# Performance work log

Measured on AMD Instinct MI355X. Metric: run time of the kernel, lower is better.

The kernel has to match this reference:

```python
import jax, jax.numpy as jnp
import numpy as np

B, T, C, H = 2, 2048, 1024, 16
D = C // H

def setup_inputs() -> dict:
    key = jax.random.key(0)
    ks = jax.random.split(key, 8)
    s = 1.0 / np.sqrt(C)
    return {
        "x": jax.random.normal(ks[0], (B, T, C), dtype=jnp.float32),
        "Wk": jax.random.normal(ks[1], (C, C), dtype=jnp.float32) * s,
        "Wq": jax.random.normal(ks[2], (C, C), dtype=jnp.float32) * s,
        "bq": jax.random.normal(ks[3], (C,), dtype=jnp.float32) * 0.02,
        "Wv": jax.random.normal(ks[4], (C, C), dtype=jnp.float32) * s,
        "bv": jax.random.normal(ks[5], (C,), dtype=jnp.float32) * 0.02,
        "Wo": jax.random.normal(ks[6], (C, C), dtype=jnp.float32) * s,
        "bo": jax.random.normal(ks[7], (C,), dtype=jnp.float32) * 0.02,
    }

def reference(x, Wk, Wq, bq, Wv, bv, Wo, bo):
    b, t, c = x.shape
    # projections (key has no bias, matching nn.Linear(bias=False))
    q = (x @ Wq.T + bq).reshape(b, t, H, D).transpose(0, 2, 1, 3)  # [B,H,T,D]
    k = (x @ Wk.T).reshape(b, t, H, D).transpose(0, 2, 1, 3)
    v = (x @ Wv.T + bv).reshape(b, t, H, D).transpose(0, 2, 1, 3)
    scale = D ** -0.5
    attn = jnp.einsum('bhqd,bhkd->bhqk', q, k) * scale  # [B,H,T,T]
    causal = jnp.tril(jnp.ones((t, t), dtype=bool))
    attn = jnp.where(causal[None, None], attn, -jnp.inf)
    attn = jax.nn.softmax(attn, axis=-1)
    y = jnp.einsum('bhqk,bhkd->bhqd', attn, v)  # [B,H,T,D]
    y = y.transpose(0, 2, 1, 3).reshape(b, t, c)
    return y @ Wo.T + bo
```

## Files before the change

### kernel.cpp

```cpp
#include <hip/hip_runtime.h>
#include <hip/hip_bf16.h>
#include <stdint.h>

#define B_ 2
#define T_ 2048
#define C_ 1024
#define H_ 16
#define D_ 64
#define M_ (B_ * T_)

typedef __bf16 bf16x8 __attribute__((ext_vector_type(8)));
typedef float f32x4 __attribute__((ext_vector_type(4)));
typedef float f32x16 __attribute__((ext_vector_type(16)));

__device__ inline void gload_lds16(const void* g, void* l) {
  __builtin_amdgcn_global_load_lds(
      (const __attribute__((address_space(1))) void*)g,
      (__attribute__((address_space(3))) void*)l, 16, 0, 0);
}

__global__ __launch_bounds__(256) void cvt_all(
    const float* __restrict__ x, const float* __restrict__ Wq,
    const float* __restrict__ Wk, const float* __restrict__ Wv,
    const float* __restrict__ Wo, __hip_bfloat16* __restrict__ xb,
    __hip_bfloat16* __restrict__ wqb, __hip_bfloat16* __restrict__ wkb,
    __hip_bfloat16* __restrict__ wvb, __hip_bfloat16* __restrict__ wob) {
  size_t t = (size_t)blockIdx.x * 256 + threadIdx.x;
  size_t e = t * 4;
  const float* src;
  __hip_bfloat16* dst;
  size_t off;
  if (e < 4194304) {
    src = x; dst = xb; off = e;
  } else {
    size_t u = e - 4194304;
    int seg = (int)(u >> 20);
    off = u & 1048575;
    src = (seg == 0) ? Wq : (seg == 1) ? Wk : (seg == 2) ? Wv : Wo;
    dst = (seg == 0) ? wqb : (seg == 1) ? wkb : (seg == 2) ? wvb : wob;
  }
  float4 v = *(const float4*)(src + off);
  union { __hip_bfloat16 h[4]; ushort4 u4; } cv;
  cv.h[0] = __float2bfloat16(v.x);
  cv.h[1] = __float2bfloat16(v.y);
  cv.h[2] = __float2bfloat16(v.z);
  cv.h[3] = __float2bfloat16(v.w);
  *(ushort4*)(dst + off) = cv.u4;
}

__global__ __launch_bounds__(256) void gemm_qkv(
    const __hip_bfloat16* __restrict__ X,
    const __hip_bfloat16* __restrict__ Wq,
    const __hip_bfloat16* __restrict__ Wk,
    const __hip_bfloat16* __restrict__ Wv,
    const float* __restrict__ bq, const float* __restrict__ bv,
    __hip_bfloat16* __restrict__ Qo, __hip_bfloat16* __restrict__ Ko,
    __hip_bfloat16* __restrict__ VTo) {
  const int z = blockIdx.z;
  const int bx = ((blockIdx.x & 3) << 3) | (blockIdx.x >> 2);
  const __hip_bfloat16* Amat;
  const __hip_bfloat16* Bmat;
  int bm, bn;
  if (z == 2) {
    Amat = Wv; Bmat = X; bm = blockIdx.y; bn = bx;
  } else {
    Amat = X; Bmat = (z == 0) ? Wq : Wk; bm = bx; bn = blockIdx.y;
  }

  const int tid = threadIdx.x;
  const int w = tid >> 6, lane = tid & 63;
  const int wr = w >> 1, wc = w & 1;
  const int lrow = lane & 15, lk = (lane >> 4) * 8;

  __shared__ __hip_bfloat16 As[128 * 32];
  __shared__ __hip_bfloat16 Bs[128 * 32];

  f32x4 acc[4][4];
#pragma unroll
  for (int m = 0; m < 4; ++m)
#pragma unroll
    for (int n = 0; n < 4; ++n) acc[m][n] = (f32x4){0.f, 0.f, 0.f, 0.f};

  for (int k0 = 0; k0 < C_; k0 += 32) {
#pragma unroll
    for (int it = 0; it < 2; ++it) {
      int e = it * 2048 + w * 512 + lane * 8;
      int row = e >> 5, col = e & 31;
      gload_lds16(Amat + (size_t)(bm * 128 + row) * C_ + k0 + col, &As[e]);
      gload_lds16(Bmat + (size_t)(bn * 128 + row) * C_ + k0 + col, &Bs[e]);
    }
    asm volatile("s_waitcnt vmcnt(0)" ::: "memory");
    __syncthreads();

    bf16x8 af[4], bfr[4];
#pragma unroll
    for (int m = 0; m < 4; ++m)
      af[m] = *(const bf16x8*)&As[(wr * 64 + m * 16 + lrow) * 32 + lk];
#pragma unroll
    for (int n = 0; n < 4; ++n)
      bfr[n] = *(const bf16x8*)&Bs[(wc * 64 + n * 16 + lrow) * 32 + lk];
#pragma unroll
    for (int m = 0; m < 4; ++m)
#pragma unroll
      for (int n = 0; n < 4; ++n)
        acc[m][n] = __builtin_amdgcn_mfma_f32_16x16x32_bf16(af[m], bfr[n],
                                                            acc[m][n], 0, 0, 0);
    __syncthreads();
  }

#pragma unroll
  for (int m = 0; m < 4; ++m) {
#pragma unroll
    for (int n = 0; n < 4; ++n) {
      f32x4 v = acc[m][n];
      int rowm = bm * 128 + wr * 64 + m * 16 + (lane >> 4) * 4;
      int coln = bn * 128 + wc * 64 + n * 16 + (lane & 15);
      if (z == 2) {
        int b = coln >> 11, tl = coln & 2047;
#pragma unroll
        for (int r = 0; r < 4; ++r) {
          int rc = rowm + r;
          int h = rc >> 6, d = rc & 63;
          VTo[(((size_t)(b * H_ + h)) * D_ + d) * T_ + tl] =
              __float2bfloat16(v[r] + bv[rc]);
        }
      } else {
        float bb = (z == 0) ? bq[coln] : 0.f;
        float sc = (z == 0) ? 0.18033688011112042f : 1.0f;
        int h = coln >> 6, d = coln & 63;
        __hip_bfloat16* Out = (z == 0) ? Qo : Ko;
#pragma unroll
        for (int r = 0; r < 4; ++r) {
          int row = rowm + r;
          int b = row >> 11, t = row & 2047;
          Out[(((size_t)(b * H_ + h)) * T_ + t) * D_ + d] =
              __float2bfloat16((v[r] + bb) * sc);
        }
      }
    }
  }
}

__global__ __launch_bounds__(256) void gemm_out(
    const __hip_bfloat16* __restrict__ X,
    const __hip_bfloat16* __restrict__ W,
    const float* __restrict__ bias, float* __restrict__ Out) {
  const int bm = ((blockIdx.x & 3) << 3) | (blockIdx.x >> 2);
  const int bn = blockIdx.y;
  const int tid = threadIdx.x;
  const int w = tid >> 6, lane = tid & 63;
  const int wr = w >> 1, wc = w & 1;
  const int lrow = lane & 15, lk = (lane >> 4) * 8;

  __shared__ __hip_bfloat16 As[128 * 32];
  __shared__ __hip_bfloat16 Bs[128 * 32];

  f32x4 acc[4][4];
#pragma unroll
  for (int m = 0; m < 4; ++m)
#pragma unroll
    for (int n = 0; n < 4; ++n) acc[m][n] = (f32x4){0.f, 0.f, 0.f, 0.f};

  for (int k0 = 0; k0 < C_; k0 += 32) {
#pragma unroll
    for (int it = 0; it < 2; ++it) {
      int e = it * 2048 + w * 512 + lane * 8;
      int row = e >> 5, col = e & 31;
      gload_lds16(X + (size_t)(bm * 128 + row) * C_ + k0 + col, &As[e]);
      gload_lds16(W + (size_t)(bn * 128 + row) * C_ + k0 + col, &Bs[e]);
    }
    asm volatile("s_waitcnt vmcnt(0)" ::: "memory");
    __syncthreads();

    bf16x8 af[4], bfr[4];
#pragma unroll
    for (int m = 0; m < 4; ++m)
      af[m] = *(const bf16x8*)&As[(wr * 64 + m * 16 + lrow) * 32 + lk];
#pragma unroll
    for (int n = 0; n < 4; ++n)
      bfr[n] = *(const bf16x8*)&Bs[(wc * 64 + n * 16 + lrow) * 32 + lk];
#pragma unroll
    for (int m = 0; m < 4; ++m)
#pragma unroll
      for (int n = 0; n < 4; ++n)
        acc[m][n] = __builtin_amdgcn_mfma_f32_16x16x32_bf16(af[m], bfr[n],
                                                            acc[m][n], 0, 0, 0);
    __syncthreads();
  }

#pragma unroll
  for (int m = 0; m < 4; ++m) {
#pragma unroll
    for (int n = 0; n < 4; ++n) {
      f32x4 v = acc[m][n];
      int coln = bn * 128 + wc * 64 + n * 16 + (lane & 15);
      float bb = bias[coln];
#pragma unroll
      for (int r = 0; r < 4; ++r) {
        int row = bm * 128 + wr * 64 + m * 16 + (lane >> 4) * 4 + r;
        Out[(size_t)row * C_ + coln] = v[r] + bb;
      }
    }
  }
}

#define MASKV_ -1e30f
#define MFLOOR_ -30000.0f
#define THR2_ 11.54f

__global__ __launch_bounds__(512, 2) void attn_fwd(
    const __hip_bfloat16* __restrict__ Q, const __hip_bfloat16* __restrict__ K,
    const __hip_bfloat16* __restrict__ VT, __hip_bfloat16* __restrict__ Y) {
  const int bh = blockIdx.x;
  const int j = blockIdx.y;
  const int tid = threadIdx.x;
  const int wid = tid >> 6, lane = tid & 63;
  const int g = wid >> 2, wq = wid & 3;
  const int hi = lane >> 5, q32 = lane & 31;
  const size_t base = (size_t)bh * T_ * D_;
  const int b = bh >> 4, hh = bh & 15;

  __shared__ __hip_bfloat16 Ks[2][2][64][64];
  __shared__ __hip_bfloat16 Vts[2][2][64][64];
  __shared__ float Sml[2][4][2][32];
  __shared__ float Om[4][32][68];

  const int gt = tid & 255;
  const int srow = gt >> 3, scnk = gt & 7;
  const int swz = (scnk ^ (srow & 7)) * 8;

#define STAGE(buf, kt)                                                      \
  {                                                                         \
    _Pragma("unroll") for (int h2 = 0; h2 < 2; ++h2) {                      \
      int row = srow + 32 * h2;                                             \
      gload_lds16(K + base + (size_t)((kt)*64 + row) * D_ + swz,            \
                  &Ks[g][(buf)][row][scnk * 8]);                            \
      gload_lds16(VT + base + (size_t)row * T_ + (kt)*64 + swz,             \
                  &Vts[g][(buf)][row][scnk * 8]);                           \
    }                                                                       \
  }

  for (int ph = 0; ph < 2; ++ph) {
    const int qt = ph ? (15 - j) : j;
    const int qg = qt * 128 + wq * 32 + q32;

    bf16x8 qf[4];
#pragma unroll
    for (int dk = 0; dk < 4; ++dk)
      qf[dk] = *(const bf16x8*)&Q[base + (size_t)qg * D_ + dk * 16 + hi * 8];

    f32x16 o0 = {}, o1 = {};
    float m_run = MFLOOR_, l_run = 0.f;

    STAGE(0, g);
    asm volatile("s_waitcnt vmcnt(0)" ::: "memory");
    __syncthreads();

    int cur = 0;
    for (int s = 0; s <= qt; ++s) {
      const int kt = 2 * s + g;
      if (s < qt) STAGE(cur ^ 1, 2 * (s + 1) + g);

      f32x16 st0 = {}, st1 = {};
      __builtin_amdgcn_s_setprio(1);
#pragma unroll
      for (int dk = 0; dk < 4; ++dk) {
        int off = (dk * 16 + hi * 8) ^ ((lane & 7) << 3);
        bf16x8 a0 = *(const bf16x8*)&Ks[g][cur][q32][off];
        bf16x8 a1 = *(const bf16x8*)&Ks[g][cur][q32 + 32][off];
        st0 = __builtin_amdgcn_mfma_f32_32x32x16_bf16(a0, qf[dk], st0, 0, 0, 0);
        st1 = __builtin_amdgcn_mfma_f32_32x32x16_bf16(a1, qf[dk], st1, 0, 0, 0);
      }
      __builtin_amdgcn_s_setprio(0);

      float sc[32];
#pragma unroll
      for (int r = 0; r < 16; ++r) {
        sc[r] = st0[r];
        sc[16 + r] = st1[r];
      }
      if (s == qt) {
#pragma unroll
        for (int r = 0; r < 16; ++r) {
          int kvl = (r & 3) + 8 * (r >> 2) + 4 * hi;
          if (kt * 64 + kvl > qg) sc[r] = MASKV_;
          if (kt * 64 + 32 + kvl > qg) sc[16 + r] = MASKV_;
        }
      }
      float mt = sc[0];
#pragma unroll
      for (int r = 1; r < 32; ++r) mt = fmaxf(mt, sc[r]);
      mt = fmaxf(mt, __shfl_xor(mt, 32));
      if (__any(mt - m_run > THR2_)) {
        float m_new = fmaxf(m_run, mt);
        float alpha = __builtin_exp2f(m_run - m_new);
        m_run = m_new;
        l_run *= alpha;
#pragma unroll
        for (int r = 0; r < 16; ++r) {
          o0[r] *= alpha;
          o1[r] *= alpha;
        }
      }
      float ls = 0.f;
#pragma unroll
      for (int r = 0; r < 32; ++r) {
        float p = __builtin_exp2f(sc[r] - m_run);
        sc[r] = p;
        ls += p;
      }
      ls += __shfl_xor(ls, 32);
      l_run += ls;

      __builtin_amdgcn_s_setprio(1);
#pragma unroll
      for (int ks = 0; ks < 4; ++ks) {
        union { unsigned w[4]; bf16x8 v; } pa;
        unsigned A, Bb;
        asm("v_cvt_pk_bf16_f32 %0, %1, %2"
            : "=v"(A) : "v"(sc[ks * 8 + 0]), "v"(sc[ks * 8 + 1]));
        asm("v_cvt_pk_bf16_f32 %0, %1, %2"
            : "=v"(Bb) : "v"(sc[ks * 8 + 4]), "v"(sc[ks * 8 + 5]));
        asm volatile("v_permlane32_swap_b32 %0, %1" : "+v"(A), "+v"(Bb));
        pa.w[0] = A;
        pa.w[2] = Bb;
        asm("v_cvt_pk_bf16_f32 %0, %1, %2"
            : "=v"(A) : "v"(sc[ks * 8 + 2]), "v"(sc[ks * 8 + 3]));
        asm("v_cvt_pk_bf16_f32 %0, %1, %2"
            : "=v"(Bb) : "v"(sc[ks * 8 + 6]), "v"(sc[ks * 8 + 7]));
        asm volatile("v_permlane32_swap_b32 %0, %1" : "+v"(A), "+v"(Bb));
        pa.w[1] = A;
        pa.w[3] = Bb;

        int voff = (ks * 16 + hi * 8) ^ ((lane & 7) << 3);
        bf16x8 v0 = *(const bf16x8*)&Vts[g][cur][q32][voff];
        bf16x8 v1 = *(const bf16x8*)&Vts[g][cur][q32 + 32][voff];
        o0 = __builtin_amdgcn_mfma_f32_32x32x16_bf16(v0, pa.v, o0, 0, 0, 0);
        o1 = __builtin_amdgcn_mfma_f32_32x32x16_bf16(v1, pa.v, o1, 0, 0, 0);
      }
      __builtin_amdgcn_s_setprio(0);

      asm volatile("s_waitcnt vmcnt(0)" ::: "memory");
      __syncthreads();
      cur ^= 1;
    }

    if (lane < 32) {
      Sml[g][wq][0][lane] = m_run;
      Sml[g][wq][1][lane] = l_run;
    }
    __syncthreads();
    float mo = Sml[1 - g][wq][0][q32];
    float lo_ = Sml[1 - g][wq][1][q32];
    float mstar = fmaxf(m_run, mo);
    float f = __builtin_exp2f(m_run - mstar);
    float fo = __builtin_exp2f(mo - mstar);
    float lstar = l_run * f + lo_ * fo;

    if (g == 1) {
#pragma unroll
      for (int dt = 0; dt < 2; ++dt) {
#pragma unroll
        for (int grp = 0; grp < 4; ++grp) {
          int dbase = grp * 8 + hi * 4 + dt * 32;
          float4 t4;
          t4.x = (dt ? o1[grp * 4 + 0] : o0[grp * 4 + 0]) * f;
          t4.y = (dt ? o1[grp * 4 + 1] : o0[grp * 4 + 1]) * f;
          t4.z = (dt ? o1[grp * 4 + 2] : o0[grp * 4 + 2]) * f;
          t4.w = (dt ? o1[grp * 4 + 3] : o0[grp * 4 + 3]) * f;
          *(float4*)&Om[wq][q32][dbase] = t4;
        }
      }
    }
    __syncthreads();
    if (g == 0) {
      float inv = 1.0f / lstar;
#pragma unroll
      for (int dt = 0; dt < 2; ++dt) {
#pragma unroll
        for (int grp = 0; grp < 4; ++grp) {
          int dbase = grp * 8 + hi * 4 + dt * 32;
          float4 m4 = *(float4*)&Om[wq][q32][dbase];
          union { __hip_bfloat16 h4[4]; ushort4 u; } pk;
          float e0 = (dt ? o1[grp * 4 + 0] : o0[grp * 4 + 0]) * f + m4.x;
          float e1 = (dt ? o1[grp * 4 + 1] : o0[grp * 4 + 1]) * f + m4.y;
          float e2 = (dt ? o1[grp * 4 + 2] : o0[grp * 4 + 2]) * f + m4.z;
          float e3 = (dt ? o1[grp * 4 + 3] : o0[grp * 4 + 3]) * f + m4.w;
          pk.h4[0] = __float2bfloat16(e0 * inv);
          pk.h4[1] = __float2bfloat16(e1 * inv);
          pk.h4[2] = __float2bfloat16(e2 * inv);
          pk.h4[3] = __float2bfloat16(e3 * inv);
          *(ushort4*)&Y[((size_t)b * T_ + qg) * C_ + hh * 64 + dbase] = pk.u;
        }
      }
    }
    __syncthreads();
  }
}

extern "C" void kernel_launch(void* const* d_in, const int* in_sizes, int n_in,
                              void* d_out, int out_size, void* d_ws,
                              size_t ws_size, hipStream_t stream) {
  const float* x = (const float*)d_in[0];
  const float* Wk = (const float*)d_in[1];
  const float* Wq = (const float*)d_in[2];
  const float* bq = (const float*)d_in[3];
  const float* Wv = (const float*)d_in[4];
  const float* bv = (const float*)d_in[5];
  const float* Wo = (const float*)d_in[6];
  const float* bo = (const float*)d_in[7];
  float* out = (float*)d_out;

  char* ws = (char*)d_ws;
  __hip_bfloat16* xb = (__hip_bfloat16*)(ws);
  __hip_bfloat16* wqb = (__hip_bfloat16*)(ws + (8ull << 20));
  __hip_bfloat16* wkb = (__hip_bfloat16*)(ws + (10ull << 20));
  __hip_bfloat16* wvb = (__hip_bfloat16*)(ws + (12ull << 20));
  __hip_bfloat16* wob = (__hip_bfloat16*)(ws + (14ull << 20));
  __hip_bfloat16* Qb = (__hip_bfloat16*)(ws + (16ull << 20));
  __hip_bfloat16* Kb = (__hip_bfloat16*)(ws + (24ull << 20));
  __hip_bfloat16* VTb = (__hip_bfloat16*)(ws + (32ull << 20));
  __hip_bfloat16* Yb = (__hip_bfloat16*)(ws + (40ull << 20));

  cvt_all<<<8192, 256, 0, stream>>>(x, Wq, Wk, Wv, Wo, xb, wqb, wkb, wvb, wob);
  gemm_qkv<<<dim3(32, 8, 3), 256, 0, stream>>>(xb, wqb, wkb, wvb, bq, bv, Qb,
                                               Kb, VTb);
  attn_fwd<<<dim3(32, 8), 512, 0, stream>>>(Qb, Kb, VTb, Yb);
  gemm_out<<<dim3(32, 8), 256, 0, stream>>>(Yb, wob, bo, out);
}
```

Baseline: 111.9 us.

## Deepen GEMM K-tiles with swizzled LDS and simplify attention to one tile per block

Both GEMM kernels now stage 64-wide K slices into LDS with an XOR swizzle and run two MFMA sub-steps per barrier. This halves the number of synchronisations and global-to-LDS rounds and avoids LDS bank conflicts. The attention kernel drops the two-group split-K design with its paired query tiles and LDS merge. Instead it launches 512 blocks of 256 threads, each handling one query tile with heavy tiles scheduled first, so the cross-group merge and its barriers disappear. In exchange, load balance now depends on the scheduler taking longest-first ordering, and each block walks the full causal KV range serially.

```diff
diff --git a/kernel.cpp b/kernel.cpp
--- a/kernel.cpp
+++ b/kernel.cpp
@@ -72,8 +72,8 @@
   const int wr = w >> 1, wc = w & 1;
   const int lrow = lane & 15, lk = (lane >> 4) * 8;
 
-  __shared__ __hip_bfloat16 As[128 * 32];
-  __shared__ __hip_bfloat16 Bs[128 * 32];
+  __shared__ __hip_bfloat16 As[128 * 64];
+  __shared__ __hip_bfloat16 Bs[128 * 64];
 
   f32x4 acc[4][4];
 #pragma unroll
@@ -81,30 +81,39 @@
 #pragma unroll
     for (int n = 0; n < 4; ++n) acc[m][n] = (f32x4){0.f, 0.f, 0.f, 0.f};
 
-  for (int k0 = 0; k0 < C_; k0 += 32) {
-#pragma unroll
-    for (int it = 0; it < 2; ++it) {
-      int e = it * 2048 + w * 512 + lane * 8;
-      int row = e >> 5, col = e & 31;
-      gload_lds16(Amat + (size_t)(bm * 128 + row) * C_ + k0 + col, &As[e]);
-      gload_lds16(Bmat + (size_t)(bn * 128 + row) * C_ + k0 + col, &Bs[e]);
+  const int scnk = tid & 7;
+  for (int k0 = 0; k0 < C_; k0 += 64) {
+#pragma unroll
+    for (int it = 0; it < 4; ++it) {
+      int e = it * 2048 + tid * 8;
+      int row = e >> 6;
+      int scol = (scnk ^ (row & 7)) * 8;
+      gload_lds16(Amat + (size_t)(bm * 128 + row) * C_ + k0 + scol, &As[e]);
+      gload_lds16(Bmat + (size_t)(bn * 128 + row) * C_ + k0 + scol, &Bs[e]);
     }
     asm volatile("s_waitcnt vmcnt(0)" ::: "memory");
     __syncthreads();
 
-    bf16x8 af[4], bfr[4];
-#pragma unroll
-    for (int m = 0; m < 4; ++m)
-      af[m] = *(const bf16x8*)&As[(wr * 64 + m * 16 + lrow) * 32 + lk];
-#pragma unroll
-    for (int n = 0; n < 4; ++n)
-      bfr[n] = *(const bf16x8*)&Bs[(wc * 64 + n * 16 + lrow) * 32 + lk];
-#pragma unroll
-    for (int m = 0; m < 4; ++m)
-#pragma unroll
-      for (int n = 0; n < 4; ++n)
-        acc[m][n] = __builtin_amdgcn_mfma_f32_16x16x32_bf16(af[m], bfr[n],
-                                                            acc[m][n], 0, 0, 0);
+#pragma unroll
+    for (int ks = 0; ks < 2; ++ks) {
+      bf16x8 af[4], bfr[4];
+#pragma unroll
+      for (int m = 0; m < 4; ++m) {
+        int R = wr * 64 + m * 16 + lrow;
+        af[m] = *(const bf16x8*)&As[R * 64 + ((ks * 32 + lk) ^ ((R & 7) << 3))];
+      }
+#pragma unroll
+      for (int n = 0; n < 4; ++n) {
+        int R = wc * 64 + n * 16 + lrow;
+        bfr[n] = *(const bf16x8*)&Bs[R * 64 + ((ks * 32 + lk) ^ ((R & 7) << 3))];
+      }
+#pragma unroll
+      for (int m = 0; m < 4; ++m)
+#pragma unroll
+        for (int n = 0; n < 4; ++n)
+          acc[m][n] = __builtin_amdgcn_mfma_f32_16x16x32_bf16(
+              af[m], bfr[n], acc[m][n], 0, 0, 0);
+    }
     __syncthreads();
   }
 
@@ -152,8 +161,8 @@
   const int wr = w >> 1, wc = w & 1;
   const int lrow = lane & 15, lk = (lane >> 4) * 8;
 
-  __shared__ __hip_bfloat16 As[128 * 32];
-  __shared__ __hip_bfloat16 Bs[128 * 32];
+  __shared__ __hip_bfloat16 As[128 * 64];
+  __shared__ __hip_bfloat16 Bs[128 * 64];
 
   f32x4 acc[4][4];
 #pragma unroll
@@ -161,30 +170,39 @@
 #pragma unroll
     for (int n = 0; n < 4; ++n) acc[m][n] = (f32x4){0.f, 0.f, 0.f, 0.f};
 
-  for (int k0 = 0; k0 < C_; k0 += 32) {
-#pragma unroll
-    for (int it = 0; it < 2; ++it) {
-      int e = it * 2048 + w * 512 + lane * 8;
-      int row = e >> 5, col = e & 31;
-      gload_lds16(X + (size_t)(bm * 128 + row) * C_ + k0 + col, &As[e]);
-      gload_lds16(W + (size_t)(bn * 128 + row) * C_ + k0 + col, &Bs[e]);
+  const int scnk = tid & 7;
+  for (int k0 = 0; k0 < C_; k0 += 64) {
+#pragma unroll
+    for (int it = 0; it < 4; ++it) {
+      int e = it * 2048 + tid * 8;
+      int row = e >> 6;
+      int scol = (scnk ^ (row & 7)) * 8;
+      gload_lds16(X + (size_t)(bm * 128 + row) * C_ + k0 + scol, &As[e]);
+      gload_lds16(W + (size_t)(bn * 128 + row) * C_ + k0 + scol, &Bs[e]);
     }
     asm volatile("s_waitcnt vmcnt(0)" ::: "memory");
     __syncthreads();
 
-    bf16x8 af[4], bfr[4];
-#pragma unroll
-    for (int m = 0; m < 4; ++m)
-      af[m] = *(const bf16x8*)&As[(wr * 64 + m * 16 + lrow) * 32 + lk];
-#pragma unroll
-    for (int n = 0; n < 4; ++n)
-      bfr[n] = *(const bf16x8*)&Bs[(wc * 64 + n * 16 + lrow) * 32 + lk];
-#pragma unroll
-    for (int m = 0; m < 4; ++m)
-#pragma unroll
-      for (int n = 0; n < 4; ++n)
-        acc[m][n] = __builtin_amdgcn_mfma_f32_16x16x32_bf16(af[m], bfr[n],
-                                                            acc[m][n], 0, 0, 0);
+#pragma unroll
+    for (int ks = 0; ks < 2; ++ks) {
+      bf16x8 af[4], bfr[4];
+#pragma unroll
+      for (int m = 0; m < 4; ++m) {
+        int R = wr * 64 + m * 16 + lrow;
+        af[m] = *(const bf16x8*)&As[R * 64 + ((ks * 32 + lk) ^ ((R & 7) << 3))];
+      }
+#pragma unroll
+      for (int n = 0; n < 4; ++n) {
+        int R = wc * 64 + n * 16 + lrow;
+        bfr[n] = *(const bf16x8*)&Bs[R * 64 + ((ks * 32 + lk) ^ ((R & 7) << 3))];
+      }
+#pragma unroll
+      for (int m = 0; m < 4; ++m)
+#pragma unroll
+        for (int n = 0; n < 4; ++n)
+          acc[m][n] = __builtin_amdgcn_mfma_f32_16x16x32_bf16(
+              af[m], bfr[n], acc[m][n], 0, 0, 0);
+    }
     __syncthreads();
   }
 
@@ -208,25 +226,21 @@
 #define MFLOOR_ -30000.0f
 #define THR2_ 11.54f
 
-__global__ __launch_bounds__(512, 2) void attn_fwd(
+__global__ __launch_bounds__(256, 4) void attn_fwd(
     const __hip_bfloat16* __restrict__ Q, const __hip_bfloat16* __restrict__ K,
     const __hip_bfloat16* __restrict__ VT, __hip_bfloat16* __restrict__ Y) {
-  const int bh = blockIdx.x;
-  const int j = blockIdx.y;
+  const int bh = blockIdx.x & 31;
+  const int qt = 15 - (blockIdx.x >> 5);
   const int tid = threadIdx.x;
-  const int wid = tid >> 6, lane = tid & 63;
-  const int g = wid >> 2, wq = wid & 3;
+  const int wq = tid >> 6, lane = tid & 63;
   const int hi = lane >> 5, q32 = lane & 31;
   const size_t base = (size_t)bh * T_ * D_;
   const int b = bh >> 4, hh = bh & 15;
 
-  __shared__ __hip_bfloat16 Ks[2][2][64][64];
-  __shared__ __hip_bfloat16 Vts[2][2][64][64];
-  __shared__ float Sml[2][4][2][32];
-  __shared__ float Om[4][32][68];
-
-  const int gt = tid & 255;
-  const int srow = gt >> 3, scnk = gt & 7;
+  __shared__ __hip_bfloat16 Ks[2][64][64];
+  __shared__ __hip_bfloat16 Vts[2][64][64];
+
+  const int srow = tid >> 3, scnk = tid & 7;
   const int swz = (scnk ^ (srow & 7)) * 8;
 
 #define STAGE(buf, kt)                                                      \
@@ -234,167 +248,131 @@
     _Pragma("unroll") for (int h2 = 0; h2 < 2; ++h2) {                      \
       int row = srow + 32 * h2;                                             \
       gload_lds16(K + base + (size_t)((kt)*64 + row) * D_ + swz,            \
-                  &Ks[g][(buf)][row][scnk * 8]);                            \
+                  &Ks[(buf)][row][scnk * 8]);                               \
       gload_lds16(VT + base + (size_t)row * T_ + (kt)*64 + swz,             \
-                  &Vts[g][(buf)][row][scnk * 8]);                           \
+                  &Vts[(buf)][row][scnk * 8]);                              \
     }                                                                       \
   }
 
-  for (int ph = 0; ph < 2; ++ph) {
-    const int qt = ph ? (15 - j) : j;
-    const int qg = qt * 128 + wq * 32 + q32;
-
-    bf16x8 qf[4];
-#pragma unroll
-    for (int dk = 0; dk < 4; ++dk)
-      qf[dk] = *(const bf16x8*)&Q[base + (size_t)qg * D_ + dk * 16 + hi * 8];
-
-    f32x16 o0 = {}, o1 = {};
-    float m_run = MFLOOR_, l_run = 0.f;
-
-    STAGE(0, g);
+  const int qg = qt * 128 + wq * 32 + q32;
+
+  bf16x8 qf[4];
+#pragma unroll
+  for (int dk = 0; dk < 4; ++dk)
+    qf[dk] = *(const bf16x8*)&Q[base + (size_t)qg * D_ + dk * 16 + hi * 8];
+
+  f32x16 o0 = {}, o1 = {};
+  float m_run = MFLOOR_, l_run = 0.f;
+
+  STAGE(0, 0);
+  asm volatile("s_waitcnt vmcnt(0)" ::: "memory");
+  __syncthreads();
+
+  const int nkt = 2 * qt + 2;
+  for (int kt = 0; kt < nkt; ++kt) {
+    const int cur = kt & 1;
+    if (kt + 1 < nkt) STAGE(cur ^ 1, kt + 1);
+
+    f32x16 st0 = {}, st1 = {};
+    __builtin_amdgcn_s_setprio(1);
+#pragma unroll
+    for (int dk = 0; dk < 4; ++dk) {
+      int off = (dk * 16 + hi * 8) ^ ((lane & 7) << 3);
+      bf16x8 a0 = *(const bf16x8*)&Ks[cur][q32][off];
+      bf16x8 a1 = *(const bf16x8*)&Ks[cur][q32 + 32][off];
+      st0 = __builtin_amdgcn_mfma_f32_32x32x16_bf16(a0, qf[dk], st0, 0, 0, 0);
+      st1 = __builtin_amdgcn_mfma_f32_32x32x16_bf16(a1, qf[dk], st1, 0, 0, 0);
+    }
+    __builtin_amdgcn_s_setprio(0);
+
+    float sc[32];
+#pragma unroll
+    for (int r = 0; r < 16; ++r) {
+      sc[r] = st0[r];
+      sc[16 + r] = st1[r];
+    }
+    if (kt >= 2 * qt) {
+#pragma unroll
+      for (int r = 0; r < 16; ++r) {
+        int kvl = (r & 3) + 8 * (r >> 2) + 4 * hi;
+        if (kt * 64 + kvl > qg) sc[r] = MASKV_;
+        if (kt * 64 + 32 + kvl > qg) sc[16 + r] = MASKV_;
+      }
+    }
+    float mt = sc[0];
+#pragma unroll
+    for (int r = 1; r < 32; ++r) mt = fmaxf(mt, sc[r]);
+    mt = fmaxf(mt, __shfl_xor(mt, 32));
+    if (__any(mt - m_run > THR2_)) {
+      float m_new = fmaxf(m_run, mt);
+      float alpha = __builtin_exp2f(m_run - m_new);
+      m_run = m_new;
+      l_run *= alpha;
+#pragma unroll
+      for (int r = 0; r < 16; ++r) {
+        o0[r] *= alpha;
+        o1[r] *= alpha;
+      }
+    }
+    float ls = 0.f;
+#pragma unroll
+    for (int r = 0; r < 32; ++r) {
+      float p = __builtin_exp2f(sc[r] - m_run);
+      sc[r] = p;
+      ls += p;
+    }
+    ls += __shfl_xor(ls, 32);
+    l_run += ls;
+
+    __builtin_amdgcn_s_setprio(1);
+#pragma unroll
+    for (int ks = 0; ks < 4; ++ks) {
+      union { unsigned w[4]; bf16x8 v; } pa;
+      unsigned A, Bb;
+      asm("v_cvt_pk_bf16_f32 %0, %1, %2"
+          : "=v"(A) : "v"(sc[ks * 8 + 0]), "v"(sc[ks * 8 + 1]));
+      asm("v_cvt_pk_bf16_f32 %0, %1, %2"
+          : "=v"(Bb) : "v"(sc[ks * 8 + 4]), "v"(sc[ks * 8 + 5]));
+      asm volatile("v_permlane32_swap_b32 %0, %1" : "+v"(A), "+v"(Bb));
+      pa.w[0] = A;
+      pa.w[2] = Bb;
+      asm("v_cvt_pk_bf16_f32 %0, %1, %2"
+          : "=v"(A) : "v"(sc[ks * 8 + 2]), "v"(sc[ks * 8 + 3]));
+      asm("v_cvt_pk_bf16_f32 %0, %1, %2"
+          : "=v"(Bb) : "v"(sc[ks * 8 + 6]), "v"(sc[ks * 8 + 7]));
+      asm volatile("v_permlane32_swap_b32 %0, %1" : "+v"(A), "+v"(Bb));
+      pa.w[1] = A;
+      pa.w[3] = Bb;
+
+      int voff = (ks * 16 + hi * 8) ^ ((lane & 7) << 3);
+      bf16x8 v0 = *(const bf16x8*)&Vts[cur][q32][voff];
+      bf16x8 v1 = *(const bf16x8*)&Vts[cur][q32 + 32][voff];
+      o0 = __builtin_amdgcn_mfma_f32_32x32x16_bf16(v0, pa.v, o0, 0, 0, 0);
+      o1 = __builtin_amdgcn_mfma_f32_32x32x16_bf16(v1, pa.v, o1, 0, 0, 0);
+    }
+    __builtin_amdgcn_s_setprio(0);
+
     asm volatile("s_waitcnt vmcnt(0)" ::: "memory");
     __syncthreads();
-
-    int cur = 0;
-    for (int s = 0; s <= qt; ++s) {
-      const int kt = 2 * s + g;
-      if (s < qt) STAGE(cur ^ 1, 2 * (s + 1) + g);
-
-      f32x16 st0 = {}, st1 = {};
-      __builtin_amdgcn_s_setprio(1);
-#pragma unroll
-      for (int dk = 0; dk < 4; ++dk) {
-        int off = (dk * 16 + hi * 8) ^ ((lane & 7) << 3);
-        bf16x8 a0 = *(const bf16x8*)&Ks[g][cur][q32][off];
-        bf16x8 a1 = *(const bf16x8*)&Ks[g][cur][q32 + 32][off];
-        st0 = __builtin_amdgcn_mfma_f32_32x32x16_bf16(a0, qf[dk], st0, 0, 0, 0);
-        st1 = __builtin_amdgcn_mfma_f32_32x32x16_bf16(a1, qf[dk], st1, 0, 0, 0);
-      }
-      __builtin_amdgcn_s_setprio(0);
-
-      float sc[32];
-#pragma unroll
-      for (int r = 0; r < 16; ++r) {
-        sc[r] = st0[r];
-        sc[16 + r] = st1[r];
-      }
-      if (s == qt) {
-#pragma unroll
-        for (int r = 0; r < 16; ++r) {
-          int kvl = (r & 3) + 8 * (r >> 2) + 4 * hi;
-          if (kt * 64 + kvl > qg) sc[r] = MASKV_;
-          if (kt * 64 + 32 + kvl > qg) sc[16 + r] = MASKV_;
-        }
-      }
-      float mt = sc[0];
-#pragma unroll
-      for (int r = 1; r < 32; ++r) mt = fmaxf(mt, sc[r]);
-      mt = fmaxf(mt, __shfl_xor(mt, 32));
-      if (__any(mt - m_run > THR2_)) {
-        float m_new = fmaxf(m_run, mt);
-        float alpha = __builtin_exp2f(m_run - m_new);
-        m_run = m_new;
-        l_run *= alpha;
-#pragma unroll
-        for (int r = 0; r < 16; ++r) {
-          o0[r] *= alpha;
-          o1[r] *= alpha;
-        }
-      }
-      float ls = 0.f;
-#pragma unroll
-      for (int r = 0; r < 32; ++r) {
-        float p = __builtin_exp2f(sc[r] - m_run);
-        sc[r] = p;
-        ls += p;
-      }
-      ls += __shfl_xor(ls, 32);
-      l_run += ls;
-
-      __builtin_amdgcn_s_setprio(1);
-#pragma unroll
-      for (int ks = 0; ks < 4; ++ks) {
-        union { unsigned w[4]; bf16x8 v; } pa;
-        unsigned A, Bb;
-        asm("v_cvt_pk_bf16_f32 %0, %1, %2"
-            : "=v"(A) : "v"(sc[ks * 8 + 0]), "v"(sc[ks * 8 + 1]));
-        asm("v_cvt_pk_bf16_f32 %0, %1, %2"
-            : "=v"(Bb) : "v"(sc[ks * 8 + 4]), "v"(sc[ks * 8 + 5]));
-        asm volatile("v_permlane32_swap_b32 %0, %1" : "+v"(A), "+v"(Bb));
-        pa.w[0] = A;
-        pa.w[2] = Bb;
-        asm("v_cvt_pk_bf16_f32 %0, %1, %2"
-            : "=v"(A) : "v"(sc[ks * 8 + 2]), "v"(sc[ks * 8 + 3]));
-        asm("v_cvt_pk_bf16_f32 %0, %1, %2"
-            : "=v"(Bb) : "v"(sc[ks * 8 + 6]), "v"(sc[ks * 8 + 7]));
-        asm volatile("v_permlane32_swap_b32 %0, %1" : "+v"(A), "+v"(Bb));
-        pa.w[1] = A;
-        pa.w[3] = Bb;
-
-        int voff = (ks * 16 + hi * 8) ^ ((lane & 7) << 3);
-        bf16x8 v0 = *(const bf16x8*)&Vts[g][cur][q32][voff];
-        bf16x8 v1 = *(const bf16x8*)&Vts[g][cur][q32 + 32][voff];
-        o0 = __builtin_amdgcn_mfma_f32_32x32x16_bf16(v0, pa.v, o0, 0, 0, 0);
-        o1 = __builtin_amdgcn_mfma_f32_32x32x16_bf16(v1, pa.v, o1, 0, 0, 0);
-      }
-      __builtin_amdgcn_s_setprio(0);
-
-      asm volatile("s_waitcnt vmcnt(0)" ::: "memory");
-      __syncthreads();
-      cur ^= 1;
-    }
-
-    if (lane < 32) {
-      Sml[g][wq][0][lane] = m_run;
-      Sml[g][wq][1][lane] = l_run;
-    }
-    __syncthreads();
-    float mo = Sml[1 - g][wq][0][q32];
-    float lo_ = Sml[1 - g][wq][1][q32];
-    float mstar = fmaxf(m_run, mo);
-    float f = __builtin_exp2f(m_run - mstar);
-    float fo = __builtin_exp2f(mo - mstar);
-    float lstar = l_run * f + lo_ * fo;
-
-    if (g == 1) {
-#pragma unroll
-      for (int dt = 0; dt < 2; ++dt) {
-#pragma unroll
-        for (int grp = 0; grp < 4; ++grp) {
-          int dbase = grp * 8 + hi * 4 + dt * 32;
-          float4 t4;
-          t4.x = (dt ? o1[grp * 4 + 0] : o0[grp * 4 + 0]) * f;
-          t4.y = (dt ? o1[grp * 4 + 1] : o0[grp * 4 + 1]) * f;
-          t4.z = (dt ? o1[grp * 4 + 2] : o0[grp * 4 + 2]) * f;
-          t4.w = (dt ? o1[grp * 4 + 3] : o0[grp * 4 + 3]) * f;
-          *(float4*)&Om[wq][q32][dbase] = t4;
-        }
-      }
-    }
-    __syncthreads();
-    if (g == 0) {
-      float inv = 1.0f / lstar;
-#pragma unroll
-      for (int dt = 0; dt < 2; ++dt) {
-#pragma unroll
-        for (int grp = 0; grp < 4; ++grp) {
-          int dbase = grp * 8 + hi * 4 + dt * 32;
-          float4 m4 = *(float4*)&Om[wq][q32][dbase];
-          union { __hip_bfloat16 h4[4]; ushort4 u; } pk;
-          float e0 = (dt ? o1[grp * 4 + 0] : o0[grp * 4 + 0]) * f + m4.x;
-          float e1 = (dt ? o1[grp * 4 + 1] : o0[grp * 4 + 1]) * f + m4.y;
-          float e2 = (dt ? o1[grp * 4 + 2] : o0[grp * 4 + 2]) * f + m4.z;
-          float e3 = (dt ? o1[grp * 4 + 3] : o0[grp * 4 + 3]) * f + m4.w;
-          pk.h4[0] = __float2bfloat16(e0 * inv);
-          pk.h4[1] = __float2bfloat16(e1 * inv);
-          pk.h4[2] = __float2bfloat16(e2 * inv);
-          pk.h4[3] = __float2bfloat16(e3 * inv);
-          *(ushort4*)&Y[((size_t)b * T_ + qg) * C_ + hh * 64 + dbase] = pk.u;
-        }
-      }
-    }
-    __syncthreads();
+  }
+
+  float inv = 1.0f / l_run;
+#pragma unroll
+  for (int dt = 0; dt < 2; ++dt) {
+#pragma unroll
+    for (int grp = 0; grp < 4; ++grp) {
+      int dbase = grp * 8 + hi * 4 + dt * 32;
+      union { __hip_bfloat16 h4[4]; ushort4 u; } pk;
+      float e0 = (dt ? o1[grp * 4 + 0] : o0[grp * 4 + 0]) * inv;
+      float e1 = (dt ? o1[grp * 4 + 1] : o0[grp * 4 + 1]) * inv;
+      float e2 = (dt ? o1[grp * 4 + 2] : o0[grp * 4 + 2]) * inv;
+      float e3 = (dt ? o1[grp * 4 + 3] : o0[grp * 4 + 3]) * inv;
+      pk.h4[0] = __float2bfloat16(e0);
+      pk.h4[1] = __float2bfloat16(e1);
+      pk.h4[2] = __float2bfloat16(e2);
+      pk.h4[3] = __float2bfloat16(e3);
+      *(ushort4*)&Y[((size_t)b * T_ + qg) * C_ + hh * 64 + dbase] = pk.u;
+    }
   }
 }
 
@@ -425,6 +403,6 @@
   cvt_all<<<8192, 256, 0, stream>>>(x, Wq, Wk, Wv, Wo, xb, wqb, wkb, wvb, wob);
   gemm_qkv<<<dim3(32, 8, 3), 256, 0, stream>>>(xb, wqb, wkb, wvb, bq, bv, Qb,
                                                Kb, VTb);
-  attn_fwd<<<dim3(32, 8), 512, 0, stream>>>(Qb, Kb, VTb, Yb);
+  attn_fwd<<<512, 256, 0, stream>>>(Qb, Kb, VTb, Yb);
   gemm_out<<<dim3(32, 8), 256, 0, stream>>>(Yb, wob, bo, out);
 }
```

After: 135.0 us. 1.21x slower.
